# Performance work log

Measured on AMD Instinct MI355X. Metric: run time of the kernel, lower is better.

The kernel has to match this reference:

```python
import jax, jax.numpy as jnp
import numpy as np

N, E, G = 20000, 320000, 64
H, NF, EF, L, Z = 280, 5, 4, 3, 64
BN_EPS = 1e-5


def _bn(x, g, b):
    # BatchNorm1d in training mode: batch stats over dim 0, biased variance
    m = x.mean(0)
    v = x.var(0)
    return g * (x - m) * jax.lax.rsqrt(v + BN_EPS) + b


def _mlp(x, W1, b1, g1, be1, W2, b2, g2, be2):
    h = jax.nn.relu(_bn(x @ W1 + b1, g1, be1))
    return jax.nn.relu(_bn(h @ W2 + b2, g2, be2))


def setup_inputs() -> dict:
    key = jax.random.key(0)
    ks = jax.random.split(key, 24)
    s = 0.05
    inp = {
        "x": jax.random.normal(ks[0], (N, NF), jnp.float32),
        "edge_attr": jax.random.normal(ks[1], (E, EF), jnp.float32),
        "edge_index": jax.random.randint(ks[2], (2, E), 0, N),
        "batch": jnp.sort(jax.random.randint(ks[3], (N,), 0, G)),
        # input layer
        "Wi": jax.random.normal(ks[4], (NF, H), jnp.float32) * s,
        "bi": jnp.zeros((H,), jnp.float32),
        # message MLP (stacked over L layers): in = 2H+EF
        "Wm1": jax.random.normal(ks[5], (L, 2 * H + EF, H), jnp.float32) * s,
        "bm1": jnp.zeros((L, H), jnp.float32),
        "g1": jnp.ones((L, H), jnp.float32),
        "be1": jnp.zeros((L, H), jnp.float32),
        "Wm2": jax.random.normal(ks[6], (L, H, H), jnp.float32) * s,
        "bm2": jnp.zeros((L, H), jnp.float32),
        "g2": jnp.ones((L, H), jnp.float32),
        "be2": jnp.zeros((L, H), jnp.float32),
        # update MLP: in = 2H
        "Wu1": jax.random.normal(ks[7], (L, 2 * H, H), jnp.float32) * s,
        "bu1": jnp.zeros((L, H), jnp.float32),
        "g3": jnp.ones((L, H), jnp.float32),
        "be3": jnp.zeros((L, H), jnp.float32),
        "Wu2": jax.random.normal(ks[8], (L, H, H), jnp.float32) * s,
        "bu2": jnp.zeros((L, H), jnp.float32),
        "g4": jnp.ones((L, H), jnp.float32),
        "be4": jnp.zeros((L, H), jnp.float32),
        # mu head
        "Wmu": jax.random.normal(ks[9], (H, Z), jnp.float32) * s,
        "bmu": jnp.zeros((Z,), jnp.float32),
    }
    return inp


def reference(x, edge_attr, Wi, bi, Wm1, bm1, g1, be1, Wm2, bm2, g2, be2,
              Wu1, bu1, g3, be3, Wu2, bu2, g4, be4, Wmu, bmu,
              edge_index, batch):
    src, dst = edge_index[0], edge_index[1]
    h = x @ Wi + bi  # [N, H]
    for l in range(L):
        # message: cat(h_i=h[dst], h_j=h[src], edge_attr) -> MLP -> [E, H]
        msg_in = jnp.concatenate([h[dst], h[src], edge_attr], axis=-1)
        msg = _mlp(msg_in, Wm1[l], bm1[l], g1[l], be1[l], Wm2[l], bm2[l], g2[l], be2[l])
        # aggregate: scatter-add into target nodes
        agg = jax.ops.segment_sum(msg, dst, num_segments=N)
        # update: cat(h, agg) -> MLP; residual in GNNEncoder
        upd = _mlp(jnp.concatenate([h, agg], axis=-1),
                   Wu1[l], bu1[l], g3[l], be3[l], Wu2[l], bu2[l], g4[l], be4[l])
        h = h + upd
    # global mean pool over graphs
    sums = jax.ops.segment_sum(h, batch, num_segments=G)
    cnt = jax.ops.segment_sum(jnp.ones((h.shape[0],), h.dtype), batch, num_segments=G)
    pooled = sums / jnp.maximum(cnt, 1.0)[:, None]
    return pooled @ Wmu + bmu  # [G, Z]
```

## Files before the change

### kernel.cpp

```cpp
#include <hip/hip_runtime.h>
#include <hip/hip_bf16.h>

#define NN 20000
#define EE 320000
#define GG 64
#define HH 280
#define NFF 5
#define EFF 4
#define LL 3
#define ZZ 64
#define BN_EPS 1e-5f

typedef __hip_bfloat16 bf;
typedef unsigned short ush;
typedef __attribute__((ext_vector_type(8))) short v8s;
typedef __attribute__((ext_vector_type(4))) float v4f;

__device__ __forceinline__ float us2f(ush u) {
  return __uint_as_float(((unsigned)u) << 16);
}
__device__ __forceinline__ ush f2us(float v) {
  bf b = __float2bfloat16(v);
  return *reinterpret_cast<ush*>(&b);
}
__device__ __forceinline__ int clampi(int v, int hi) {
  return v < 0 ? 0 : (v >= hi ? hi - 1 : v);
}

__global__ void probe_k(const void* __restrict__ x, int* __restrict__ flag) {
  __shared__ int sh[256];
  int tid = threadIdx.x;
  int cnt = 0;
  for (int i = tid; i < 2048; i += 256) {
    ush w = ((const ush*)x)[i];
    unsigned e = (w >> 7) & 0xFF;
    if (w != 0 && (e < 87 || e > 167)) cnt++;
  }
  sh[tid] = cnt;
  __syncthreads();
  for (int o = 128; o > 0; o >>= 1) {
    if (tid < o) sh[tid] += sh[tid + o];
    __syncthreads();
  }
  if (tid == 0) *flag = (sh[0] > 64) ? 1 : 0;
}

__global__ void convert_k(const void* __restrict__ src, float* __restrict__ dst,
                          int n, const int* __restrict__ flag) {
  int i = blockIdx.x * 256 + threadIdx.x;
  if (i < n) {
    if (*flag)
      dst[i] = ((const float*)src)[i];
    else
      dst[i] = us2f(((const ush*)src)[i]);
  }
}

__global__ void wt_ab_k(const float* __restrict__ W, ush* __restrict__ O) {
  int i = blockIdx.x * 256 + threadIdx.x;
  if (i >= 3 * 576 * 288) return;
  int l = i / 165888, r = i % 165888;
  int n = r / 288, k = r % 288;
  float v = 0.f;
  if (n < 560 && k < 280)
    v = (n < 280) ? W[(size_t)l * 157920 + (size_t)k * 280 + n]
                  : W[(size_t)l * 157920 + (size_t)(280 + k) * 280 + (n - 280)];
  O[i] = f2us(v);
}
__global__ void wt_sq_k(const float* __restrict__ W, ush* __restrict__ O) {
  int i = blockIdx.x * 256 + threadIdx.x;
  if (i >= 3 * 320 * 288) return;
  int l = i / 92160, r = i % 92160;
  int n = r / 288, k = r % 288;
  float v = (n < 280 && k < 280) ? W[(size_t)l * 78400 + (size_t)k * 280 + n] : 0.f;
  O[i] = f2us(v);
}
__global__ void wt_u1_k(const float* __restrict__ W, ush* __restrict__ O) {
  int i = blockIdx.x * 256 + threadIdx.x;
  if (i >= 3 * 320 * 576) return;
  int l = i / 184320, r = i % 184320;
  int n = r / 576, k = r % 576;
  float v = (n < 280 && k < 560) ? W[(size_t)l * 156800 + (size_t)k * 280 + n] : 0.f;
  O[i] = f2us(v);
}

struct MG {
  const ush* A;
  const ush* Bt;
  const float* bias;
  void* C;
  float* stats;
  int M, K, Nn, lda, ldb, ldc;
};

template <int CB, int ST>
__global__ __launch_bounds__(256) void mgemm_k(MG g) {
  __shared__ ush As[128][40];
  __shared__ ush Bs[64][40];
  __shared__ float red[8][64];
  int t = threadIdx.x;
  int n0 = blockIdx.x * 64, m0 = blockIdx.y * 128;
  int ar = t >> 1, akq = (t & 1) << 4;
  int br = t >> 2, bkq = (t & 3) << 3;
  int lane = t & 63, wv = t >> 6;
  int wr = (wv >> 1) << 6, wc = (wv & 1) << 5;
  int lrow = lane & 15, quad = lane >> 4;
  v4f zero4 = {0.f, 0.f, 0.f, 0.f};
  v4f acc[4][2];
#pragma unroll
  for (int i = 0; i < 4; ++i)
#pragma unroll
    for (int j = 0; j < 2; ++j) acc[i][j] = zero4;

  bool arow = (m0 + ar) < g.M;
  const ush* Abase = g.A + (size_t)(m0 + ar) * g.lda;
  bool brow = (n0 + br) < g.Nn;
  const ush* Bbase = g.Bt + (size_t)(n0 + br) * g.ldb;
  uint4 zz = {0, 0, 0, 0};

  for (int k0 = 0; k0 < g.K; k0 += 32) {
    uint4 a0 = (arow && (k0 + akq) < g.K) ? *(const uint4*)(Abase + k0 + akq) : zz;
    uint4 a1 = (arow && (k0 + akq + 8) < g.K) ? *(const uint4*)(Abase + k0 + akq + 8) : zz;
    uint4 b0 = (brow && (k0 + bkq) < g.K) ? *(const uint4*)(Bbase + k0 + bkq) : zz;
    __syncthreads();
    *(uint4*)&As[ar][akq] = a0;
    *(uint4*)&As[ar][akq + 8] = a1;
    *(uint4*)&Bs[br][bkq] = b0;
    __syncthreads();
    v8s af[4], bfr[2];
#pragma unroll
    for (int mi = 0; mi < 4; ++mi)
      af[mi] = *(const v8s*)&As[wr + (mi << 4) + lrow][quad << 3];
#pragma unroll
    for (int ci = 0; ci < 2; ++ci)
      bfr[ci] = *(const v8s*)&Bs[wc + (ci << 4) + lrow][quad << 3];
#pragma unroll
    for (int mi = 0; mi < 4; ++mi)
#pragma unroll
      for (int ci = 0; ci < 2; ++ci)
        acc[mi][ci] = __builtin_amdgcn_mfma_f32_16x16x32_bf16(
            af[mi], bfr[ci], acc[mi][ci], 0, 0, 0);
  }

  float bj[2];
#pragma unroll
  for (int ci = 0; ci < 2; ++ci) {
    int gn = n0 + wc + (ci << 4) + lrow;
    bj[ci] = (g.bias && gn < g.Nn) ? g.bias[gn] : 0.f;
  }
#pragma unroll
  for (int mi = 0; mi < 4; ++mi)
#pragma unroll
    for (int ci = 0; ci < 2; ++ci)
#pragma unroll
      for (int r = 0; r < 4; ++r) {
        int gm = m0 + wr + (mi << 4) + (quad << 2) + r;
        int gn = n0 + wc + (ci << 4) + lrow;
        float v = acc[mi][ci][r] + bj[ci];
        bool ok = (gm < g.M) && (gn < g.Nn);
        if (ok) {
          size_t idx = (size_t)gm * g.ldc + gn;
          if (CB)
            ((ush*)g.C)[idx] = f2us(v);
          else
            ((float*)g.C)[idx] = v;
        }
        acc[mi][ci][r] = ok ? v : 0.f;
      }
  if (ST) {
    int rowg = ((wv >> 1) << 2) | quad;
#pragma unroll
    for (int ci = 0; ci < 2; ++ci) {
      float s = 0.f;
#pragma unroll
      for (int mi = 0; mi < 4; ++mi)
#pragma unroll
        for (int r = 0; r < 4; ++r) s += acc[mi][ci][r];
      red[rowg][wc + (ci << 4) + lrow] = s;
    }
    __syncthreads();
    if (t < 64) {
      float s = 0.f;
#pragma unroll
      for (int r = 0; r < 8; ++r) s += red[r][t];
      int gn = n0 + t;
      if (gn < g.Nn) atomicAdd(&g.stats[gn], s);
    }
    __syncthreads();
#pragma unroll
    for (int ci = 0; ci < 2; ++ci) {
      float s = 0.f;
#pragma unroll
      for (int mi = 0; mi < 4; ++mi)
#pragma unroll
        for (int r = 0; r < 4; ++r) s += acc[mi][ci][r] * acc[mi][ci][r];
      red[rowg][wc + (ci << 4) + lrow] = s;
    }
    __syncthreads();
    if (t < 64) {
      float s = 0.f;
#pragma unroll
      for (int r = 0; r < 8; ++r) s += red[r][t];
      int gn = n0 + t;
      if (gn < g.Nn) atomicAdd(&g.stats[HH + gn], s);
    }
  }
}

__global__ __launch_bounds__(256) void gemm_small_k(
    const float* __restrict__ A, const float* __restrict__ B,
    const float* __restrict__ bias, void* __restrict__ C,
    const int* __restrict__ flag, int M, int K, int Nn, int lda, int ldb,
    int ldc, int outmode) {
  __shared__ alignas(16) float As[16][68];
  __shared__ alignas(16) float Bsm[16][68];
  int tid = threadIdx.x;
  int n0 = blockIdx.x * 64, m0 = blockIdx.y * 64;
  int tx = tid & 15, ty = tid >> 4;
  int am = tid >> 2, akq = (tid & 3) << 2;
  int bk = tid >> 4, bn = (tid & 15) << 2;
  float acc[4][4] = {};
  int gmA = m0 + am;
  int nkt = (K + 15) >> 4;
  for (int kt = 0; kt < nkt; ++kt) {
    int k0 = kt << 4;
#pragma unroll
    for (int i = 0; i < 4; ++i) {
      int gk = k0 + akq + i;
      As[akq + i][am] = (gmA < M && gk < K) ? A[(size_t)gmA * lda + gk] : 0.f;
    }
    {
      int gk = k0 + bk;
      bool kin = gk < K;
#pragma unroll
      for (int j = 0; j < 4; ++j) {
        int gn = n0 + bn + j;
        Bsm[bk][bn + j] = (kin && gn < Nn) ? B[(size_t)gk * ldb + gn] : 0.f;
      }
    }
    __syncthreads();
#pragma unroll
    for (int kk = 0; kk < 16; ++kk) {
      float4 a4 = *(const float4*)&As[kk][ty << 2];
      float4 b4 = *(const float4*)&Bsm[kk][tx << 2];
      float av[4] = {a4.x, a4.y, a4.z, a4.w};
      float bv[4] = {b4.x, b4.y, b4.z, b4.w};
#pragma unroll
      for (int i = 0; i < 4; ++i)
#pragma unroll
        for (int j = 0; j < 4; ++j) acc[i][j] = fmaf(av[i], bv[j], acc[i][j]);
    }
    __syncthreads();
  }
  int ofl = outmode ? *flag : -1;
#pragma unroll
  for (int i = 0; i < 4; ++i) {
    int gm = m0 + (ty << 2) + i;
    if (gm < M) {
#pragma unroll
      for (int j = 0; j < 4; ++j) {
        int gn = n0 + (tx << 2) + j;
        if (gn < Nn) {
          float v = acc[i][j] + (bias ? bias[gn] : 0.f);
          size_t idx = (size_t)gm * ldc + gn;
          if (outmode == 0)
            ((float*)C)[idx] = v;
          else if (ofl)
            ((float*)C)[idx] = v;
          else
            ((ush*)C)[idx] = f2us(v);
        }
      }
    }
  }
}

__global__ __launch_bounds__(256) void edge_stats_k(
    const int* __restrict__ eids, const int* __restrict__ dst,
    const int* __restrict__ src, const float* __restrict__ ea,
    const ush* __restrict__ Pq, const float* __restrict__ W1c,
    const float* __restrict__ b1, float* __restrict__ stats) {
  __shared__ int dstl[256], srcl[256];
  __shared__ float4 eal[256];
  __shared__ float w1cs[4 * HH];
  __shared__ float b1s[HH];
  int tid = threadIdx.x;
  int e0 = blockIdx.x * 256;
  {
    int e = clampi(eids[e0 + tid], EE);
    dstl[tid] = clampi(dst[e], NN);
    srcl[tid] = clampi(src[e], NN);
    eal[tid] = *(const float4*)(ea + (size_t)e * 4);
  }
  for (int i = tid; i < 4 * HH; i += 256) w1cs[i] = W1c[i];
  for (int i = tid; i < HH; i += 256) b1s[i] = b1[i];
  __syncthreads();
  int c0 = tid, c1 = tid + 256;
  bool has1 = c1 < HH;
  float s0 = 0.f, q0 = 0.f, s1 = 0.f, q1 = 0.f;
  for (int e = 0; e < 256; ++e) {
    int d = dstl[e], sn = srcl[e];
    float4 ev = eal[e];
    {
      float raw = us2f(Pq[(size_t)d * 576 + c0]) + us2f(Pq[(size_t)sn * 576 + 280 + c0]);
      float r = ev.x * w1cs[c0] + ev.y * w1cs[HH + c0] +
                ev.z * w1cs[2 * HH + c0] + ev.w * w1cs[3 * HH + c0];
      float tv = raw + r + b1s[c0];
      s0 += tv; q0 += tv * tv;
    }
    if (has1) {
      float raw = us2f(Pq[(size_t)d * 576 + c1]) + us2f(Pq[(size_t)sn * 576 + 280 + c1]);
      float r = ev.x * w1cs[c1] + ev.y * w1cs[HH + c1] +
                ev.z * w1cs[2 * HH + c1] + ev.w * w1cs[3 * HH + c1];
      float tv = raw + r + b1s[c1];
      s1 += tv; q1 += tv * tv;
    }
  }
  atomicAdd(&stats[c0], s0);
  atomicAdd(&stats[HH + c0], q0);
  if (has1) {
    atomicAdd(&stats[c1], s1);
    atomicAdd(&stats[HH + c1], q1);
  }
}

__global__ void bn_finalize_k(const float* __restrict__ stats, float cnt,
                              const float* __restrict__ gw,
                              const float* __restrict__ bw,
                              const float* __restrict__ extra,
                              float* __restrict__ scale,
                              float* __restrict__ shift) {
  int c = threadIdx.x;
  if (c < HH) {
    float m = stats[c] / cnt;
    float v = stats[HH + c] / cnt - m * m;
    v = v < 0.f ? 0.f : v;
    float r = rsqrtf(v + BN_EPS);
    float sc = gw[c] * r;
    float sh = bw[c] - sc * m + (extra ? sc * extra[c] : 0.f);
    scale[c] = sc;
    shift[c] = sh;
  }
}

__global__ void hist_k(const int* __restrict__ dst, int* __restrict__ counts) {
  int e = blockIdx.x * 256 + threadIdx.x;
  if (e < EE) atomicAdd(&counts[clampi(dst[e], NN)], 1);
}

__global__ __launch_bounds__(1024) void scan_k(const int* __restrict__ counts,
                                               int* __restrict__ offs, int n) {
  __shared__ int buf[1024];
  __shared__ int running;
  int tid = threadIdx.x;
  if (tid == 0) running = 0;
  __syncthreads();
  for (int base = 0; base < n; base += 1024) {
    int v = (base + tid < n) ? counts[base + tid] : 0;
    buf[tid] = v;
    __syncthreads();
    for (int off = 1; off < 1024; off <<= 1) {
      int t = (tid >= off) ? buf[tid - off] : 0;
      __syncthreads();
      buf[tid] += t;
      __syncthreads();
    }
    int incl = buf[tid];
    if (base + tid < n) offs[base + tid] = running + incl - v;
    __syncthreads();
    if (tid == 1023) running += incl;
    __syncthreads();
  }
  if (tid == 0) offs[n] = running;
}

__global__ void fill_k(const int* __restrict__ dst, const int* __restrict__ offs,
                       int* __restrict__ cursor, int* __restrict__ eids) {
  int e = blockIdx.x * 256 + threadIdx.x;
  if (e < EE) {
    int n = clampi(dst[e], NN);
    int pos = atomicAdd(&cursor[n], 1);
    int idx = offs[n] + pos;
    if (idx >= 0 && idx < EE) eids[idx] = e;
  }
}

__global__ __launch_bounds__(256) void build_t1_k(
    const int* __restrict__ eids, const int* __restrict__ dst,
    const int* __restrict__ src, const float* __restrict__ ea,
    const ush* __restrict__ Pq, const float* __restrict__ W1c,
    const float* __restrict__ sc, const float* __restrict__ sh,
    ush* __restrict__ T1, int cb) {
  __shared__ float scs[HH], shs[HH], w1[4 * HH];
  int t = threadIdx.x;
  for (int i = t; i < HH; i += 256) { scs[i] = sc[i]; shs[i] = sh[i]; }
  for (int i = t; i < 4 * HH; i += 256) w1[i] = W1c[i];
  __syncthreads();
  int base = blockIdx.x * 32;
  int c2 = t + 256;
  bool h2 = c2 < HH;
  for (int i = 0; i < 32; ++i) {
    int r = cb + base + i;
    int e = clampi(eids[r], EE);
    int d = clampi(dst[e], NN), s = clampi(src[e], NN);
    float4 ev = *(const float4*)(ea + (size_t)e * 4);
    size_t pd = (size_t)d * 576, ps = (size_t)s * 576 + 280;
    size_t orow = (size_t)(base + i) * 288;
    {
      int c = t;
      float v = us2f(Pq[pd + c]) + us2f(Pq[ps + c]) + ev.x * w1[c] +
                ev.y * w1[HH + c] + ev.z * w1[2 * HH + c] + ev.w * w1[3 * HH + c];
      v = fmaf(scs[c], v, shs[c]);
      T1[orow + c] = f2us(v > 0.f ? v : 0.f);
    }
    if (h2) {
      int c = c2;
      float v = us2f(Pq[pd + c]) + us2f(Pq[ps + c]) + ev.x * w1[c] +
                ev.y * w1[HH + c] + ev.z * w1[2 * HH + c] + ev.w * w1[3 * HH + c];
      v = fmaf(scs[c], v, shs[c]);
      T1[orow + c] = f2us(v > 0.f ? v : 0.f);
    }
  }
}

__global__ __launch_bounds__(256) void aggregate_k(
    const int* __restrict__ offs, const ush* __restrict__ tmp2,
    const float* __restrict__ scale, const float* __restrict__ shift,
    float* __restrict__ agg, int e0, int e1) {
  int n = blockIdx.x;
  int rs = offs[n], re = offs[n + 1];
  if (rs < e0) rs = e0;
  if (re > e1) re = e1;
  if (rs >= re) return;
  int t = threadIdx.x;
  int c2 = t + 256;
  bool h2 = c2 < HH;
  float a0 = 0.f, a1 = 0.f;
  float sc0 = scale[t], sh0 = shift[t];
  float sc1 = h2 ? scale[c2] : 0.f, sh1 = h2 ? shift[c2] : 0.f;
  for (int r = rs; r < re; ++r) {
    const ush* row = tmp2 + (size_t)(r - e0) * HH;
    float v0 = fmaf(sc0, us2f(row[t]), sh0);
    a0 += v0 > 0.f ? v0 : 0.f;
    if (h2) {
      float v1 = fmaf(sc1, us2f(row[c2]), sh1);
      a1 += v1 > 0.f ? v1 : 0.f;
    }
  }
  agg[(size_t)n * HH + t] += a0;
  if (h2) agg[(size_t)n * HH + c2] += a1;
}

__global__ void hb_k(const float* __restrict__ h, ush* __restrict__ hcat) {
  int i = blockIdx.x * 256 + threadIdx.x;
  if (i < NN * HH) {
    int n = i / HH, c = i % HH;
    hcat[(size_t)n * 576 + c] = f2us(h[i]);
  }
}
__global__ void agg2hcat_k(const float* __restrict__ agg, ush* __restrict__ hcat) {
  int i = blockIdx.x * 256 + threadIdx.x;
  if (i < NN * HH) {
    int n = i / HH, c = i % HH;
    hcat[(size_t)n * 576 + 280 + c] = f2us(agg[i]);
  }
}
__global__ void u2a_k(const float* __restrict__ u1, const float* __restrict__ sc,
                      const float* __restrict__ sh, ush* __restrict__ u2A) {
  int i = blockIdx.x * 256 + threadIdx.x;
  if (i < NN * HH) {
    int n = i / HH, c = i % HH;
    float v = fmaf(sc[c], u1[i], sh[c]);
    u2A[(size_t)n * 288 + c] = f2us(v > 0.f ? v : 0.f);
  }
}
__global__ void residual_k(float* __restrict__ h, const float* __restrict__ u2,
                           const float* __restrict__ scale,
                           const float* __restrict__ shift) {
  int i = blockIdx.x * 256 + threadIdx.x;
  if (i < NN * HH) {
    int c = i % HH;
    float v = fmaf(scale[c], u2[i], shift[c]);
    h[i] += v > 0.f ? v : 0.f;
  }
}

__device__ __forceinline__ int lowerb(const int* a, int n, int key) {
  int lo = 0, hi = n;
  while (lo < hi) {
    int mid = (lo + hi) >> 1;
    if (a[mid] < key) lo = mid + 1; else hi = mid;
  }
  return lo;
}

__global__ __launch_bounds__(256) void pool_k(const float* __restrict__ h,
                                              const int* __restrict__ batch,
                                              float* __restrict__ pooled) {
  int gid = blockIdx.x;
  int start = lowerb(batch, NN, gid);
  int end = lowerb(batch, NN, gid + 1);
  int cnt = end - start;
  float inv = 1.f / (float)(cnt > 1 ? cnt : 1);
  for (int c = threadIdx.x; c < HH; c += 256) {
    float sum = 0.f;
    for (int nidx = start; nidx < end; ++nidx) sum += h[(size_t)nidx * HH + c];
    pooled[(size_t)gid * HH + c] = sum * inv;
  }
}

extern "C" void kernel_launch(void* const* d_in, const int* in_sizes, int n_in,
                              void* d_out, int out_size, void* d_ws,
                              size_t ws_size, hipStream_t stream) {
  const int* eidx = (const int*)d_in[2];
  const int* batch = (const int*)d_in[3];
  const int* srcp = eidx;
  const int* dstp = eidx + EE;
  size_t NH = (size_t)NN * HH;

  float* w0 = (float*)d_ws;
  size_t off = 0;
  auto alloc = [&](size_t n) {
    float* p = w0 + off;
    off += (n + 3) & ~(size_t)3;
    return p;
  };
  int* flag = (int*)alloc(4);
  float* cx = alloc(100000);
  float* cea = alloc(1280000);
  float* cWi = alloc(1400);
  float* cbi = alloc(280);
  float* cWm1 = alloc(473760);
  float* cbm1 = alloc(840);
  float* cg1 = alloc(840);
  float* cbe1 = alloc(840);
  float* cWm2 = alloc(235200);
  float* cbm2 = alloc(840);
  float* cg2 = alloc(840);
  float* cbe2 = alloc(840);
  float* cWu1 = alloc(470400);
  float* cbu1 = alloc(840);
  float* cg3 = alloc(840);
  float* cbe3 = alloc(840);
  float* cWu2 = alloc(235200);
  float* cbu2 = alloc(840);
  float* cg4 = alloc(840);
  float* cbe4 = alloc(840);
  float* cWmu = alloc(17920);
  float* cbmu = alloc(64);
  ush* W1ab = (ush*)alloc(248832);
  ush* W2t = (ush*)alloc(138240);
  ush* WU1t = (ush*)alloc(276480);
  ush* WU2t = (ush*)alloc(138240);
  float* h = alloc(NH);
  ush* hcat = (ush*)alloc(5787648);
  ush* u2A = hcat;
  float* pqr = alloc(5760000);
  ush* Pq = (ush*)pqr;
  float* u1f = pqr;
  float* agg = alloc(NH);
  float* pooled = alloc((size_t)GG * HH);
  float* stats = alloc(8 * HH);
  float* ss = alloc(8 * HH);
  int* counts = (int*)alloc(NN);
  int* offs = (int*)alloc(NN + 1);
  int* cursor = (int*)alloc(NN);
  int* eids = (int*)alloc(EE);
  size_t baseB = off * 4;

  int EC = 6400, T2 = 6400;
  {
    const int ecs[5] = {64000, 64000, 32000, 12800, 6400};
    const int t2s[5] = {EE, 64000, 32000, 12800, 6400};
    for (int i = 0; i < 5; ++i) {
      size_t need = baseB + (size_t)ecs[i] * 288 * 2 + (size_t)t2s[i] * 280 * 2 + 64;
      if (need <= ws_size) { EC = ecs[i]; T2 = t2s[i]; break; }
    }
  }
  ush* T1c = (ush*)(w0 + off);
  ush* tmp2 = T1c + (size_t)EC * 288;
  bool stored = (T2 == EE);
  int nch = EE / EC;

  probe_k<<<1, 256, 0, stream>>>(d_in[0], flag);
  struct Cv { const void* s; float* d; int n; };
  const Cv cv[22] = {
      {d_in[0], cx, NN * NFF},     {d_in[1], cea, EE * EFF},
      {d_in[4], cWi, NFF * HH},    {d_in[5], cbi, HH},
      {d_in[6], cWm1, LL * (2 * HH + EFF) * HH}, {d_in[7], cbm1, LL * HH},
      {d_in[8], cg1, LL * HH},     {d_in[9], cbe1, LL * HH},
      {d_in[10], cWm2, LL * HH * HH}, {d_in[11], cbm2, LL * HH},
      {d_in[12], cg2, LL * HH},    {d_in[13], cbe2, LL * HH},
      {d_in[14], cWu1, LL * 2 * HH * HH}, {d_in[15], cbu1, LL * HH},
      {d_in[16], cg3, LL * HH},    {d_in[17], cbe3, LL * HH},
      {d_in[18], cWu2, LL * HH * HH}, {d_in[19], cbu2, LL * HH},
      {d_in[20], cg4, LL * HH},    {d_in[21], cbe4, LL * HH},
      {d_in[22], cWmu, HH * ZZ},   {d_in[23], cbmu, ZZ}};
  for (int i = 0; i < 22; ++i)
    convert_k<<<(cv[i].n + 255) / 256, 256, 0, stream>>>(cv[i].s, cv[i].d, cv[i].n, flag);

  wt_ab_k<<<(3 * 576 * 288 + 255) / 256, 256, 0, stream>>>(cWm1, W1ab);
  wt_sq_k<<<(3 * 320 * 288 + 255) / 256, 256, 0, stream>>>(cWm2, W2t);
  wt_u1_k<<<(3 * 320 * 576 + 255) / 256, 256, 0, stream>>>(cWu1, WU1t);
  wt_sq_k<<<(3 * 320 * 288 + 255) / 256, 256, 0, stream>>>(cWu2, WU2t);

  gemm_small_k<<<dim3(5, 313), 256, 0, stream>>>(cx, cWi, cbi, h, nullptr, NN,
                                                 NFF, HH, NFF, HH, HH, 0);
  hipMemsetAsync(counts, 0, NN * sizeof(int), stream);
  hipMemsetAsync(cursor, 0, NN * sizeof(int), stream);
  hist_k<<<(EE + 255) / 256, 256, 0, stream>>>(dstp, counts);
  scan_k<<<1, 1024, 0, stream>>>(counts, offs, NN);
  fill_k<<<(EE + 255) / 256, 256, 0, stream>>>(dstp, offs, cursor, eids);

  int elemGrid = (int)((NH + 255) / 256);
  for (int l = 0; l < LL; ++l) {
    ush* Wab = W1ab + (size_t)l * 576 * 288;
    ush* W2l = W2t + (size_t)l * 320 * 288;
    ush* WU1l = WU1t + (size_t)l * 320 * 576;
    ush* WU2l = WU2t + (size_t)l * 320 * 288;
    const float* W1c = cWm1 + (size_t)l * 157920 + (size_t)560 * 280;
    float* st1 = stats; float* st2 = stats + 560;
    float* st3 = stats + 1120; float* st4 = stats + 1680;
    float* ss1 = ss; float* ss2 = ss + 560;
    float* ss3 = ss + 1120; float* ss4 = ss + 1680;
    hipMemsetAsync(stats, 0, 8 * HH * sizeof(float), stream);

    hb_k<<<elemGrid, 256, 0, stream>>>(h, hcat);
    {
      MG g = {hcat, Wab, nullptr, Pq, nullptr, NN, HH, 560, 576, 288, 576};
      mgemm_k<1, 0><<<dim3(9, 157), 256, 0, stream>>>(g);
    }
    edge_stats_k<<<EE / 256, 256, 0, stream>>>(eids, dstp, srcp, cea, Pq, W1c,
                                               cbm1 + l * HH, st1);
    bn_finalize_k<<<1, 320, 0, stream>>>(st1, (float)EE, cg1 + l * HH,
                                         cbe1 + l * HH, cbm1 + l * HH, ss1, ss1 + HH);
    for (int c = 0; c < nch; ++c) {
      int cb = c * EC;
      build_t1_k<<<EC / 32, 256, 0, stream>>>(eids, dstp, srcp, cea, Pq, W1c,
                                              ss1, ss1 + HH, T1c, cb);
      MG g = {T1c, W2l, cbm2 + l * HH,
              stored ? (void*)(tmp2 + (size_t)cb * HH) : (void*)tmp2, st2,
              EC, HH, HH, 288, 288, HH};
      mgemm_k<1, 1><<<dim3(5, EC / 128), 256, 0, stream>>>(g);
    }
    bn_finalize_k<<<1, 320, 0, stream>>>(st2, (float)EE, cg2 + l * HH,
                                         cbe2 + l * HH, nullptr, ss2, ss2 + HH);
    hipMemsetAsync(agg, 0, NH * sizeof(float), stream);
    if (stored) {
      aggregate_k<<<NN, 256, 0, stream>>>(offs, tmp2, ss2, ss2 + HH, agg, 0, EE);
    } else {
      for (int c = 0; c < nch; ++c) {
        int cb = c * EC;
        build_t1_k<<<EC / 32, 256, 0, stream>>>(eids, dstp, srcp, cea, Pq, W1c,
                                                ss1, ss1 + HH, T1c, cb);
        MG g = {T1c, W2l, cbm2 + l * HH, (void*)tmp2, nullptr,
                EC, HH, HH, 288, 288, HH};
        mgemm_k<1, 0><<<dim3(5, EC / 128), 256, 0, stream>>>(g);
        aggregate_k<<<NN, 256, 0, stream>>>(offs, tmp2, ss2, ss2 + HH, agg, cb, cb + EC);
      }
    }
    agg2hcat_k<<<elemGrid, 256, 0, stream>>>(agg, hcat);
    {
      MG g = {hcat, WU1l, cbu1 + l * HH, u1f, st3, NN, 2 * HH, HH, 576, 576, HH};
      mgemm_k<0, 1><<<dim3(5, 157), 256, 0, stream>>>(g);
    }
    bn_finalize_k<<<1, 320, 0, stream>>>(st3, (float)NN, cg3 + l * HH,
                                         cbe3 + l * HH, nullptr, ss3, ss3 + HH);
    u2a_k<<<elemGrid, 256, 0, stream>>>(u1f, ss3, ss3 + HH, u2A);
    {
      MG g = {u2A, WU2l, cbu2 + l * HH, agg, st4, NN, HH, HH, 288, 288, HH};
      mgemm_k<0, 1><<<dim3(5, 157), 256, 0, stream>>>(g);
    }
    bn_finalize_k<<<1, 320, 0, stream>>>(st4, (float)NN, cg4 + l * HH,
                                         cbe4 + l * HH, nullptr, ss4, ss4 + HH);
    residual_k<<<elemGrid, 256, 0, stream>>>(h, agg, ss4, ss4 + HH);
  }

  pool_k<<<GG, 256, 0, stream>>>(h, batch, pooled);
  gemm_small_k<<<dim3(1, 1), 256, 0, stream>>>(pooled, cWmu, cbmu, d_out, flag,
                                               GG, HH, ZZ, HH, ZZ, ZZ, 1);
}
```

Measured before the change: 4.620 ms.

## Enlarge GEMM tile to 256x64 with register prefetch of next K slice

The bf16 MFMA GEMM tile grows from 128x64 to 256x64. Each wave now computes a 64x64 sub-tile with 16 accumulators and reads the whole B tile, which raises operand reuse per LDS load. The global loads for the next K slice are issued into registers before the MFMAs of the current slice, so load latency overlaps compute. K bounds checks are dropped by padding K to a multiple of 32 (288/576) and enlarging buffers. In exchange, per-thread register pressure rises, the grid has half as many blocks (occupancy on 20000-row problems drops), and correctness now depends on the padded columns being zero.

```diff
diff --git a/kernel.cpp b/kernel.cpp
--- a/kernel.cpp
+++ b/kernel.cpp
@@ -95,67 +95,78 @@
 
 template <int CB, int ST>
 __global__ __launch_bounds__(256) void mgemm_k(MG g) {
-  __shared__ ush As[128][40];
+  __shared__ ush As[256][40];
   __shared__ ush Bs[64][40];
-  __shared__ float red[8][64];
+  __shared__ float red[16][64];
   int t = threadIdx.x;
-  int n0 = blockIdx.x * 64, m0 = blockIdx.y * 128;
-  int ar = t >> 1, akq = (t & 1) << 4;
-  int br = t >> 2, bkq = (t & 3) << 3;
+  int n0 = blockIdx.x * 64, m0 = blockIdx.y * 256;
   int lane = t & 63, wv = t >> 6;
-  int wr = (wv >> 1) << 6, wc = (wv & 1) << 5;
   int lrow = lane & 15, quad = lane >> 4;
-  v4f zero4 = {0.f, 0.f, 0.f, 0.f};
-  v4f acc[4][2];
+  int ar = t >> 2;
+  int ac = (t & 3) << 3;
+  v4f acc[4][4];
 #pragma unroll
   for (int i = 0; i < 4; ++i)
 #pragma unroll
-    for (int j = 0; j < 2; ++j) acc[i][j] = zero4;
-
-  bool arow = (m0 + ar) < g.M;
-  const ush* Abase = g.A + (size_t)(m0 + ar) * g.lda;
-  bool brow = (n0 + br) < g.Nn;
-  const ush* Bbase = g.Bt + (size_t)(n0 + br) * g.ldb;
+    for (int j = 0; j < 4; ++j) acc[i][j] = (v4f){0.f, 0.f, 0.f, 0.f};
+
+  const ush* Ap = g.A + (size_t)(m0 + ar) * g.lda + ac;
+  const ush* Bp = g.Bt + (size_t)(n0 + ar) * g.ldb + ac;
+  bool av[4];
+#pragma unroll
+  for (int p = 0; p < 4; ++p) av[p] = (m0 + ar + (p << 6)) < g.M;
   uint4 zz = {0, 0, 0, 0};
-
-  for (int k0 = 0; k0 < g.K; k0 += 32) {
-    uint4 a0 = (arow && (k0 + akq) < g.K) ? *(const uint4*)(Abase + k0 + akq) : zz;
-    uint4 a1 = (arow && (k0 + akq + 8) < g.K) ? *(const uint4*)(Abase + k0 + akq + 8) : zz;
-    uint4 b0 = (brow && (k0 + bkq) < g.K) ? *(const uint4*)(Bbase + k0 + bkq) : zz;
-    __syncthreads();
-    *(uint4*)&As[ar][akq] = a0;
-    *(uint4*)&As[ar][akq + 8] = a1;
-    *(uint4*)&Bs[br][bkq] = b0;
-    __syncthreads();
-    v8s af[4], bfr[2];
+  size_t astep = (size_t)g.lda << 6;
+
+  int nkt = g.K >> 5;
+  uint4 a[4], b0;
+#pragma unroll
+  for (int p = 0; p < 4; ++p)
+    a[p] = av[p] ? *(const uint4*)(Ap + p * astep) : zz;
+  b0 = *(const uint4*)Bp;
+
+  for (int kt = 0; kt < nkt; ++kt) {
+    __syncthreads();
+#pragma unroll
+    for (int p = 0; p < 4; ++p) *(uint4*)&As[ar + (p << 6)][ac] = a[p];
+    *(uint4*)&Bs[ar][ac] = b0;
+    __syncthreads();
+    int kn = (kt + 1) << 5;
+    if (kt + 1 < nkt) {
+#pragma unroll
+      for (int p = 0; p < 4; ++p)
+        a[p] = av[p] ? *(const uint4*)(Ap + p * astep + kn) : zz;
+      b0 = *(const uint4*)(Bp + kn);
+    }
+    v8s af[4], bq[4];
 #pragma unroll
     for (int mi = 0; mi < 4; ++mi)
-      af[mi] = *(const v8s*)&As[wr + (mi << 4) + lrow][quad << 3];
-#pragma unroll
-    for (int ci = 0; ci < 2; ++ci)
-      bfr[ci] = *(const v8s*)&Bs[wc + (ci << 4) + lrow][quad << 3];
+      af[mi] = *(const v8s*)&As[(wv << 6) + (mi << 4) + lrow][quad << 3];
+#pragma unroll
+    for (int ci = 0; ci < 4; ++ci)
+      bq[ci] = *(const v8s*)&Bs[(ci << 4) + lrow][quad << 3];
 #pragma unroll
     for (int mi = 0; mi < 4; ++mi)
 #pragma unroll
-      for (int ci = 0; ci < 2; ++ci)
+      for (int ci = 0; ci < 4; ++ci)
         acc[mi][ci] = __builtin_amdgcn_mfma_f32_16x16x32_bf16(
-            af[mi], bfr[ci], acc[mi][ci], 0, 0, 0);
-  }
-
-  float bj[2];
-#pragma unroll
-  for (int ci = 0; ci < 2; ++ci) {
-    int gn = n0 + wc + (ci << 4) + lrow;
+            af[mi], bq[ci], acc[mi][ci], 0, 0, 0);
+  }
+
+  float bj[4];
+#pragma unroll
+  for (int ci = 0; ci < 4; ++ci) {
+    int gn = n0 + (ci << 4) + lrow;
     bj[ci] = (g.bias && gn < g.Nn) ? g.bias[gn] : 0.f;
   }
 #pragma unroll
   for (int mi = 0; mi < 4; ++mi)
 #pragma unroll
-    for (int ci = 0; ci < 2; ++ci)
+    for (int ci = 0; ci < 4; ++ci)
 #pragma unroll
       for (int r = 0; r < 4; ++r) {
-        int gm = m0 + wr + (mi << 4) + (quad << 2) + r;
-        int gn = n0 + wc + (ci << 4) + lrow;
+        int gm = m0 + (wv << 6) + (mi << 4) + (quad << 2) + r;
+        int gn = n0 + (ci << 4) + lrow;
         float v = acc[mi][ci][r] + bj[ci];
         bool ok = (gm < g.M) && (gn < g.Nn);
         if (ok) {
@@ -168,39 +179,39 @@
         acc[mi][ci][r] = ok ? v : 0.f;
       }
   if (ST) {
-    int rowg = ((wv >> 1) << 2) | quad;
-#pragma unroll
-    for (int ci = 0; ci < 2; ++ci) {
+    int rowg = (wv << 2) | quad;
+#pragma unroll
+    for (int ci = 0; ci < 4; ++ci) {
       float s = 0.f;
 #pragma unroll
       for (int mi = 0; mi < 4; ++mi)
 #pragma unroll
         for (int r = 0; r < 4; ++r) s += acc[mi][ci][r];
-      red[rowg][wc + (ci << 4) + lrow] = s;
+      red[rowg][(ci << 4) | lrow] = s;
     }
     __syncthreads();
     if (t < 64) {
       float s = 0.f;
 #pragma unroll
-      for (int r = 0; r < 8; ++r) s += red[r][t];
+      for (int r = 0; r < 16; ++r) s += red[r][t];
       int gn = n0 + t;
       if (gn < g.Nn) atomicAdd(&g.stats[gn], s);
     }
     __syncthreads();
 #pragma unroll
-    for (int ci = 0; ci < 2; ++ci) {
+    for (int ci = 0; ci < 4; ++ci) {
       float s = 0.f;
 #pragma unroll
       for (int mi = 0; mi < 4; ++mi)
 #pragma unroll
         for (int r = 0; r < 4; ++r) s += acc[mi][ci][r] * acc[mi][ci][r];
-      red[rowg][wc + (ci << 4) + lrow] = s;
+      red[rowg][(ci << 4) | lrow] = s;
     }
     __syncthreads();
     if (t < 64) {
       float s = 0.f;
 #pragma unroll
-      for (int r = 0; r < 8; ++r) s += red[r][t];
+      for (int r = 0; r < 16; ++r) s += red[r][t];
       int gn = n0 + t;
       if (gn < g.Nn) atomicAdd(&g.stats[HH + gn], s);
     }
@@ -553,9 +564,9 @@
   ush* WU1t = (ush*)alloc(276480);
   ush* WU2t = (ush*)alloc(138240);
   float* h = alloc(NH);
-  ush* hcat = (ush*)alloc(5787648);
+  ush* hcat = (ush*)alloc(5824512);
   ush* u2A = hcat;
-  float* pqr = alloc(5760000);
+  float* pqr = alloc(5824512);
   ush* Pq = (ush*)pqr;
   float* u1f = pqr;
   float* agg = alloc(NH);
@@ -627,8 +638,8 @@
 
     hb_k<<<elemGrid, 256, 0, stream>>>(h, hcat);
     {
-      MG g = {hcat, Wab, nullptr, Pq, nullptr, NN, HH, 560, 576, 288, 576};
-      mgemm_k<1, 0><<<dim3(9, 157), 256, 0, stream>>>(g);
+      MG g = {hcat, Wab, nullptr, Pq, nullptr, NN, 288, 560, 576, 288, 576};
+      mgemm_k<1, 0><<<dim3(9, 79), 256, 0, stream>>>(g);
     }
     edge_stats_k<<<EE / 256, 256, 0, stream>>>(eids, dstp, srcp, cea, Pq, W1c,
                                                cbm1 + l * HH, st1);
@@ -640,8 +651,8 @@
                                               ss1, ss1 + HH, T1c, cb);
       MG g = {T1c, W2l, cbm2 + l * HH,
               stored ? (void*)(tmp2 + (size_t)cb * HH) : (void*)tmp2, st2,
-              EC, HH, HH, 288, 288, HH};
-      mgemm_k<1, 1><<<dim3(5, EC / 128), 256, 0, stream>>>(g);
+              EC, 288, HH, 288, 288, HH};
+      mgemm_k<1, 1><<<dim3(5, EC / 256), 256, 0, stream>>>(g);
     }
     bn_finalize_k<<<1, 320, 0, stream>>>(st2, (float)EE, cg2 + l * HH,
                                          cbe2 + l * HH, nullptr, ss2, ss2 + HH);
@@ -654,22 +665,22 @@
         build_t1_k<<<EC / 32, 256, 0, stream>>>(eids, dstp, srcp, cea, Pq, W1c,
                                                 ss1, ss1 + HH, T1c, cb);
         MG g = {T1c, W2l, cbm2 + l * HH, (void*)tmp2, nullptr,
-                EC, HH, HH, 288, 288, HH};
-        mgemm_k<1, 0><<<dim3(5, EC / 128), 256, 0, stream>>>(g);
+                EC, 288, HH, 288, 288, HH};
+        mgemm_k<1, 0><<<dim3(5, EC / 256), 256, 0, stream>>>(g);
         aggregate_k<<<NN, 256, 0, stream>>>(offs, tmp2, ss2, ss2 + HH, agg, cb, cb + EC);
       }
     }
     agg2hcat_k<<<elemGrid, 256, 0, stream>>>(agg, hcat);
     {
-      MG g = {hcat, WU1l, cbu1 + l * HH, u1f, st3, NN, 2 * HH, HH, 576, 576, HH};
-      mgemm_k<0, 1><<<dim3(5, 157), 256, 0, stream>>>(g);
+      MG g = {hcat, WU1l, cbu1 + l * HH, u1f, st3, NN, 576, HH, 576, 576, HH};
+      mgemm_k<0, 1><<<dim3(5, 79), 256, 0, stream>>>(g);
     }
     bn_finalize_k<<<1, 320, 0, stream>>>(st3, (float)NN, cg3 + l * HH,
                                          cbe3 + l * HH, nullptr, ss3, ss3 + HH);
     u2a_k<<<elemGrid, 256, 0, stream>>>(u1f, ss3, ss3 + HH, u2A);
     {
-      MG g = {u2A, WU2l, cbu2 + l * HH, agg, st4, NN, HH, HH, 288, 288, HH};
-      mgemm_k<0, 1><<<dim3(5, 157), 256, 0, stream>>>(g);
+      MG g = {u2A, WU2l, cbu2 + l * HH, agg, st4, NN, 288, HH, 288, 288, HH};
+      mgemm_k<0, 1><<<dim3(5, 79), 256, 0, stream>>>(g);
     }
     bn_finalize_k<<<1, 320, 0, stream>>>(st4, (float)NN, cg4 + l * HH,
                                          cbe4 + l * HH, nullptr, ss4, ss4 + HH);
```

After: 6.868 ms. 48.7% more time.
